# Optimization experiments

Measured on AMD Instinct MI355X. Metric: run time of the kernel, lower is better.

## Reference

```python
import jax, jax.numpy as jnp
import numpy as np

LN_EPS = 1e-5


def setup_inputs() -> dict:
    key = jax.random.key(0)
    ks = jax.random.split(key, 12)
    B, T, C, D, P = 4, 1024, 16, 256, 4096
    s = 1.0 / np.sqrt(D)
    x = jax.random.normal(ks[0], (B, T, C, D), jnp.float32)
    x_mask = jax.random.uniform(ks[1], (B, T, C)) < 0.1
    pos = jax.random.randint(ks[2], (B, T, C), 0, P)
    ang = jax.random.uniform(ks[3], (P, D // 2), minval=-np.pi, maxval=np.pi)
    pe = jnp.stack([jnp.cos(ang), jnp.sin(ang)], axis=-1)  # [P, D/2, 2] unit complex
    wq_w = jax.random.normal(ks[4], (D, D), jnp.float32) * s
    wq_b = jnp.zeros((D,), jnp.float32)
    wk_w = jax.random.normal(ks[5], (D, D), jnp.float32) * s
    wk_b = jnp.zeros((D,), jnp.float32)
    wv_w = jax.random.normal(ks[6], (D, D), jnp.float32) * s
    wv_b = jnp.zeros((D,), jnp.float32)
    ln_g = jnp.ones((D,), jnp.float32)
    ln_b = jnp.zeros((D,), jnp.float32)
    ls_gamma = 1e-5 * jnp.ones((D,), jnp.float32)
    return {"x": x, "x_mask": x_mask, "pos": pos, "pe": pe,
            "wq_w": wq_w, "wq_b": wq_b, "wk_w": wk_w, "wk_b": wk_b,
            "wv_w": wv_w, "wv_b": wv_b, "ln_g": ln_g, "ln_b": ln_b,
            "ls_gamma": ls_gamma}


def _rotate(q, pe, pos):
    # q: [B,T,C,D]; pe: [P,D/2,2]; pos: [B,T,C] -> complex mult q * pe[pos]
    B, T, C, D = q.shape
    qr = q.reshape(B, T, C, D // 2, 2)
    r = pe[pos]  # [B,T,C,D/2,2]
    re = qr[..., 0] * r[..., 0] - qr[..., 1] * r[..., 1]
    im = qr[..., 0] * r[..., 1] + qr[..., 1] * r[..., 0]
    return jnp.stack([re, im], axis=-1).reshape(B, T, C, D)


def reference(x, x_mask, pos, pe, wq_w, wq_b, wk_w, wk_b, wv_w, wv_b, ln_g, ln_b, ls_gamma):
    B, T, C, D = x.shape
    scale = 1.0 / jnp.sqrt(jnp.asarray(D, x.dtype))
    q = jnp.einsum('btcd,ed->btce', x, wq_w) + wq_b
    k = jnp.einsum('btcd,ed->btce', x, wk_w) + wk_b
    v = jnp.einsum('btcd,ed->btce', x, wv_w) + wv_b
    q = _rotate(q, pe, pos)
    k = _rotate(k, pe, pos)
    # (b c) t d layout -> keep as [b,c,t,d]
    q = q.transpose(0, 2, 1, 3)
    k = k.transpose(0, 2, 1, 3)
    v = v.transpose(0, 2, 1, 3)
    attn = jnp.einsum('bcqd,bckd->bcqk', q, k) * scale  # [b,c,tq,tk]
    m = x_mask.transpose(0, 2, 1)  # [b,c,t]
    mask = m[:, :, :, None] | m[:, :, None, :]  # OR-combined pad mask
    attn = jnp.where(mask, jnp.asarray(-1e30, attn.dtype), attn)
    p = jax.nn.softmax(attn, axis=-1)
    # fully masked rows: torch softmax(-inf row)->nan->nan_to_num(0)
    all_masked = jnp.all(mask, axis=-1, keepdims=True)
    p = jnp.where(all_masked, jnp.zeros((), p.dtype), p)
    o = jnp.einsum('bcqk,bckd->bqcd', p, v)  # [b,t,c,d]
    y = x + ls_gamma * o
    mu = y.mean(-1, keepdims=True)
    var = ((y - mu) ** 2).mean(-1, keepdims=True)
    out = (y - mu) / jnp.sqrt(var + LN_EPS) * ln_g + ln_b
    return out
```

## Files before the change

kernel.cpp:

```cpp
#include <hip/hip_runtime.h>


typedef __attribute__((ext_vector_type(8))) short short8_t;
typedef __attribute__((ext_vector_type(4))) short short4_t;
typedef __attribute__((ext_vector_type(8))) float float8_t;
typedef __attribute__((ext_vector_type(4))) float float4_t;
typedef __attribute__((ext_vector_type(2))) float float2_t;

__device__ __forceinline__ float b2f(short s) {
    union { unsigned int u; float f; } x;
    x.u = ((unsigned int)(unsigned short)s) << 16;
    return x.f;
}
__device__ __forceinline__ short f2bt(float f) {
    union { float f; unsigned int u; } x; x.f = f;
    return (short)(x.u >> 16);
}

__device__ __forceinline__ void stage16(const short* g, short* l) {
    __builtin_amdgcn_global_load_lds(
        (const __attribute__((address_space(1))) unsigned int*)g,
        (__attribute__((address_space(3))) unsigned int*)l, 16, 0, 0);
}

__global__ __launch_bounds__(256) void prep_kernel(
    const float* __restrict__ wq, const float* __restrict__ wk,
    const float* __restrict__ wv, const unsigned char* __restrict__ xmask,
    short* __restrict__ wb, float* __restrict__ mbg)
{
    if (blockIdx.x < 192) {
        int idx = blockIdx.x * 256 + threadIdx.x;
        int mat = idx >> 14, off = idx & 16383;
        const float* src = (mat == 0) ? wq : ((mat == 1) ? wk : wv);
        float4_t v = *(const float4_t*)(src + (long)off * 4);
        short4_t o;
#pragma unroll
        for (int j = 0; j < 4; j++) o[j] = f2bt(v[j]);
        *(short4_t*)(wb + (long)idx * 4) = o;
    } else {
        int idx = (blockIdx.x - 192) * 256 + threadIdx.x;
        int bc = idx >> 10, t = idx & 1023;
        int b = bc >> 4, c = bc & 15;
        mbg[idx] = xmask[((long)b * 1024 + t) * 16 + c] ? -1e30f : 0.0f;
    }
}

__global__ __launch_bounds__(256) void qkv_mfma_kernel(
    const float* __restrict__ x, const int* __restrict__ pos,
    const float* __restrict__ pe, const short* __restrict__ wb,
    const float* __restrict__ bq, const float* __restrict__ bk,
    const float* __restrict__ bv,
    short* __restrict__ qo, short* __restrict__ ko, short* __restrict__ vt)
{
    __shared__ __align__(16) short xs[64 * 264];
    __shared__ __align__(16) short ys[18432];
    __shared__ int posb[64];

    const int tid = threadIdx.x;
    const int lane = tid & 63;
    const int wid = tid >> 6;
    const int bc = blockIdx.x >> 4;
    const int t0 = (blockIdx.x & 15) * 64;
    const int b = bc >> 4, c = bc & 15;
    const int row = lane & 15, quad = lane >> 4;
    const int odd = lane & 1;
    const int n0 = wid * 64;
    const long kvbase = (long)bc * 262144;

#pragma unroll
    for (int j = 0; j < 8; j++) {
        int idx = tid + j * 256;
        int r = idx >> 5, c8 = idx & 31;
        const float* xp = x + (((long)b * 1024 + t0 + r) * 16 + c) * 256 + c8 * 8;
        float4_t a = *(const float4_t*)xp;
        float4_t d = *(const float4_t*)(xp + 4);
        short8_t o;
        o[0] = f2bt(a.x); o[1] = f2bt(a.y); o[2] = f2bt(a.z); o[3] = f2bt(a.w);
        o[4] = f2bt(d.x); o[5] = f2bt(d.y); o[6] = f2bt(d.z); o[7] = f2bt(d.w);
        *(short8_t*)&xs[r * 264 + c8 * 8] = o;
    }
    if (tid < 64) posb[tid] = pos[((long)b * 1024 + t0 + tid) * 16 + c];
    __syncthreads();

#pragma unroll 1
    for (int mat = 0; mat < 3; mat++) {
        const short* W = wb + mat * 65536;
        float4_t acc[4][4];
#pragma unroll
        for (int mt = 0; mt < 4; mt++)
#pragma unroll
            for (int nt = 0; nt < 4; nt++) acc[mt][nt] = (float4_t){0.f, 0.f, 0.f, 0.f};

        short8_t Ac[4], Bc[4], An[4], Bn[4];
        auto loadA = [&](short8_t* A, int k0) {
#pragma unroll
            for (int mt = 0; mt < 4; mt++)
                A[mt] = *(const short8_t*)&xs[(mt * 16 + row) * 264 + k0 * 32 + quad * 8];
        };
        auto loadB = [&](short8_t* Bf, int k0) {
#pragma unroll
            for (int nt = 0; nt < 4; nt++)
                Bf[nt] = *(const short8_t*)(W + (n0 + nt * 16 + row) * 256 + k0 * 32 + quad * 8);
        };
        loadA(Ac, 0); loadB(Bc, 0);
#pragma unroll
        for (int k0 = 0; k0 < 8; k0++) {
            if (k0 < 7) { loadA(An, k0 + 1); loadB(Bn, k0 + 1); }
#pragma unroll
            for (int mt = 0; mt < 4; mt++)
#pragma unroll
                for (int nt = 0; nt < 4; nt++)
                    acc[mt][nt] = __builtin_amdgcn_mfma_f32_16x16x32_bf16(
                        Ac[mt], Bc[nt], acc[mt][nt], 0, 0, 0);
            if (k0 < 7) {
#pragma unroll
                for (int i = 0; i < 4; i++) { Ac[i] = An[i]; Bc[i] = Bn[i]; }
            }
        }

        const float* bias = (mat == 0) ? bq : ((mat == 1) ? bk : bv);
        float bs[4];
#pragma unroll
        for (int nt = 0; nt < 4; nt++) bs[nt] = bias[n0 + nt * 16 + row];
#pragma unroll
        for (int mt = 0; mt < 4; mt++)
#pragma unroll
            for (int nt = 0; nt < 4; nt++)
#pragma unroll
                for (int r = 0; r < 4; r++) acc[mt][nt][r] += bs[nt];

        if (mat < 2) {
#pragma unroll
            for (int mt = 0; mt < 4; mt++)
#pragma unroll
                for (int r = 0; r < 4; r++) {
                    int p = posb[mt * 16 + quad * 4 + r];
                    const float* pb = pe + (long)p * 256;
#pragma unroll
                    for (int nt = 0; nt < 4; nt++) {
                        int i = (n0 + nt * 16 + row) >> 1;
                        float2_t cs = *(const float2_t*)(pb + i * 2);
                        float v = acc[mt][nt][r];
                        float pr = __shfl_xor(v, 1);
                        acc[mt][nt][r] = v * cs.x + pr * (odd ? cs.y : -cs.y);
                    }
                }
        }

        __syncthreads();
        if (mat < 2) {
#pragma unroll
            for (int mt = 0; mt < 4; mt++)
#pragma unroll
                for (int nt = 0; nt < 4; nt++) {
                    int n = n0 + nt * 16 + row;
#pragma unroll
                    for (int r = 0; r < 4; r++)
                        ys[(mt * 16 + quad * 4 + r) * 264 + n] = f2bt(acc[mt][nt][r]);
                }
            __syncthreads();
            short* dst = ((mat == 0) ? qo : ko) + kvbase + (long)t0 * 256;
#pragma unroll
            for (int j = 0; j < 8; j++) {
                int idx = tid + j * 256;
                int r = idx >> 5, c8 = idx & 31;
                *(short8_t*)(dst + r * 256 + c8 * 8) = *(const short8_t*)&ys[r * 264 + c8 * 8];
            }
        } else {
#pragma unroll
            for (int mt = 0; mt < 4; mt++)
#pragma unroll
                for (int nt = 0; nt < 4; nt++) {
                    int n = n0 + nt * 16 + row;
                    short4_t o4;
#pragma unroll
                    for (int r = 0; r < 4; r++) o4[r] = f2bt(acc[mt][nt][r]);
                    *(short4_t*)&ys[n * 72 + mt * 16 + quad * 4] = o4;
                }
            __syncthreads();
#pragma unroll
            for (int j = 0; j < 8; j++) {
                int idx = tid + j * 256;
                int d = idx >> 3, t8 = idx & 7;
                *(short8_t*)(vt + kvbase + (long)d * 1024 + t0 + t8 * 8) =
                    *(const short8_t*)&ys[d * 72 + t8 * 8];
            }
        }
    }
}

__global__ __launch_bounds__(512, 2) void attn_kernel(
    const short* __restrict__ qg, const short* __restrict__ kg,
    const short* __restrict__ vt, const float* __restrict__ mbg,
    const float* __restrict__ x,
    const float* __restrict__ lsg, const float* __restrict__ lng,
    const float* __restrict__ lnb, float* __restrict__ out)
{
    __shared__ __align__(16) short lds[56320];

    const int tid = threadIdx.x;
    const int lane = tid & 63;
    const int wid = tid >> 6;
    const int bid = (blockIdx.x & 7) * 64 + (blockIdx.x >> 3);
    const int bc = bid >> 3;
    const int tq0 = (bid & 7) * 128;
    const int b = bc >> 4, c = bc & 15;
    const long kvbase = (long)bc * 262144;
    const int bcq = bc * 1024;
    const int row = lane & 15, quad = lane >> 4;
    float* mbsf = (float*)&lds[54272];

    auto stage = [&](int j, int buf) {
#pragma unroll
        for (int i = 0; i < 2; i++) {
            int rp = (wid * 2 + i) * 2;
            int r = rp + (lane >> 5);
            int slot = lane & 31;
            const short* g = kg + kvbase + (long)(j * 32 + r) * 256 +
                             ((slot ^ (r & 7)) << 3);
            stage16(g, &lds[buf * 8192 + rp * 256]);
        }
#pragma unroll
        for (int i = 0; i < 2; i++) {
            int db = (wid * 2 + i) * 16;
            int d = db + (lane >> 2);
            int slot = lane & 3;
            const short* g = vt + kvbase + (long)d * 1024 + j * 32 +
                             (((slot ^ ((d >> 1) & 3))) << 3);
            stage16(g, &lds[24576 + buf * 8192 + db * 32]);
        }
    };

    stage(0, 0);
    stage(1, 1);
#pragma unroll
    for (int i = tid; i < 1024; i += 512) mbsf[i] = mbg[bcq + i];
    short8_t aq[8];
#pragma unroll
    for (int f = 0; f < 8; f++)
        aq[f] = *(const short8_t*)(qg + kvbase +
            (long)(tq0 + wid * 16 + row) * 256 + f * 32 + quad * 8);

    float4_t oacc[16];
#pragma unroll
    for (int nt = 0; nt < 16; nt++) oacc[nt] = (float4_t){0.f, 0.f, 0.f, 0.f};
    float m[4], lsum[4];
#pragma unroll
    for (int r = 0; r < 4; r++) { m[r] = -__builtin_inff(); lsum[r] = 0.f; }

    const float scale = 0.0625f;
    const int ptw = 49152 + wid * 640 + row * 20 + quad * 4;
    const int prd = 49152 + wid * 640 + quad * 160 + row;

    asm volatile("s_waitcnt lgkmcnt(0)" ::: "memory");

    int bcur = 0;
#pragma unroll 1
    for (int j = 0; j < 32; j++) {
        int bnx = bcur + 2; if (bnx >= 3) bnx -= 3;
        if (j < 30) {
            stage(j + 2, bnx);
            asm volatile("s_waitcnt vmcnt(8)" ::: "memory");
        } else if (j == 30) {
            asm volatile("s_waitcnt vmcnt(4)" ::: "memory");
        } else {
            asm volatile("s_waitcnt vmcnt(0)" ::: "memory");
        }
        __builtin_amdgcn_s_barrier();

        const short* Kb = &lds[bcur * 8192];
        const short* Vb = &lds[24576 + bcur * 8192];

        float4_t s0 = {0.f, 0.f, 0.f, 0.f}, s1 = {0.f, 0.f, 0.f, 0.f};
#pragma unroll
        for (int f = 0; f < 8; f++) {
            short8_t k0 = *(const short8_t*)&Kb[row * 256 + (((f * 4 + quad) ^ (row & 7)) << 3)];
            short8_t k1 = *(const short8_t*)&Kb[(16 + row) * 256 + (((f * 4 + quad) ^ ((16 + row) & 7)) << 3)];
            s0 = __builtin_amdgcn_mfma_f32_16x16x32_bf16(aq[f], k0, s0, 0, 0, 0);
            s1 = __builtin_amdgcn_mfma_f32_16x16x32_bf16(aq[f], k1, s1, 0, 0, 0);
        }
        float mb0 = mbsf[j * 32 + row], mb1 = mbsf[j * 32 + 16 + row];
        float sv[2][4], tm[4];
#pragma unroll
        for (int r = 0; r < 4; r++) {
            sv[0][r] = s0[r] * scale + mb0;
            sv[1][r] = s1[r] * scale + mb1;
            tm[r] = fmaxf(sv[0][r], sv[1][r]);
        }
#pragma unroll
        for (int r = 0; r < 4; r++)
#pragma unroll
            for (int o = 1; o < 16; o <<= 1) tm[r] = fmaxf(tm[r], __shfl_xor(tm[r], o));
        float g = fmaxf(fmaxf(tm[0] - m[0], tm[1] - m[1]),
                        fmaxf(tm[2] - m[2], tm[3] - m[3]));
        if (!__all(g <= 8.f)) {
#pragma unroll
            for (int r = 0; r < 4; r++) {
                float nm = fmaxf(m[r], tm[r]);
                float fac = __expf(m[r] - nm);
                lsum[r] *= fac; m[r] = nm;
#pragma unroll
                for (int nt = 0; nt < 16; nt++) oacc[nt][r] *= fac;
            }
        }
        short4_t p4[2];
#pragma unroll
        for (int h = 0; h < 2; h++)
#pragma unroll
            for (int r = 0; r < 4; r++) {
                float p = __expf(sv[h][r] - m[r]);
                lsum[r] += p;
                p4[h][r] = f2bt(p);
            }
        *(short4_t*)&lds[ptw] = p4[0];
        *(short4_t*)&lds[ptw + 320] = p4[1];
        short8_t pa;
#pragma unroll
        for (int jj = 0; jj < 8; jj++) pa[jj] = lds[prd + jj * 20];

#pragma unroll
        for (int nt = 0; nt < 16; nt++) {
            int d = nt * 16 + row;
            short8_t vbf = *(const short8_t*)&Vb[d * 32 + ((quad ^ ((d >> 1) & 3)) << 3)];
            oacc[nt] = __builtin_amdgcn_mfma_f32_16x16x32_bf16(pa, vbf, oacc[nt], 0, 0, 0);
        }

        asm volatile("s_waitcnt lgkmcnt(0)" ::: "memory");
        __builtin_amdgcn_s_barrier();
        bcur++; if (bcur >= 3) bcur = 0;
    }

    float inv[4];
#pragma unroll
    for (int r = 0; r < 4; r++) {
        float s = lsum[r];
#pragma unroll
        for (int o = 1; o < 16; o <<= 1) s += __shfl_xor(s, o);
        int qi = tq0 + wid * 16 + quad * 4 + r;
        inv[r] = (mbsf[qi] != 0.f) ? 0.f : (1.f / s);
    }
    long xb[4];
#pragma unroll
    for (int r = 0; r < 4; r++)
        xb[r] = (((long)b * 1024 + tq0 + wid * 16 + quad * 4 + r) * 16 + c) * 256 + row;

    float s1r[4] = {0.f, 0.f, 0.f, 0.f}, s2r[4] = {0.f, 0.f, 0.f, 0.f};
#pragma unroll
    for (int nt = 0; nt < 16; nt++) {
        int d = nt * 16 + row;
        float lg = lsg[d];
#pragma unroll
        for (int r = 0; r < 4; r++) {
            float yy = x[xb[r] + nt * 16] + lg * (oacc[nt][r] * inv[r]);
            oacc[nt][r] = yy;
            s1r[r] += yy; s2r[r] += yy * yy;
        }
    }
    float mu[4], rstd[4];
#pragma unroll
    for (int r = 0; r < 4; r++) {
#pragma unroll
        for (int o = 1; o < 16; o <<= 1) {
            s1r[r] += __shfl_xor(s1r[r], o);
            s2r[r] += __shfl_xor(s2r[r], o);
        }
        mu[r] = s1r[r] * (1.f / 256.f);
        float var = s2r[r] * (1.f / 256.f) - mu[r] * mu[r];
        rstd[r] = rsqrtf(var + 1e-5f);
    }
#pragma unroll
    for (int nt = 0; nt < 16; nt++) {
        int d = nt * 16 + row;
        float g2 = lng[d], b2 = lnb[d];
#pragma unroll
        for (int r = 0; r < 4; r++)
            out[xb[r] + nt * 16] = (oacc[nt][r] - mu[r]) * rstd[r] * g2 + b2;
    }
}

extern "C" void kernel_launch(void* const* d_in, const int* in_sizes, int n_in,
                              void* d_out, int out_size, void* d_ws, size_t ws_size,
                              hipStream_t stream) {
    const float* x = (const float*)d_in[0];
    const unsigned char* xmask = (const unsigned char*)d_in[1];
    const int* pos = (const int*)d_in[2];
    const float* pe = (const float*)d_in[3];
    const float* wq = (const float*)d_in[4];
    const float* bq = (const float*)d_in[5];
    const float* wk = (const float*)d_in[6];
    const float* bk = (const float*)d_in[7];
    const float* wv = (const float*)d_in[8];
    const float* bv = (const float*)d_in[9];
    const float* lng = (const float*)d_in[10];
    const float* lnb = (const float*)d_in[11];
    const float* lsg = (const float*)d_in[12];
    float* out = (float*)d_out;

    short* qw = (short*)d_ws;
    short* kw = qw + 16777216;
    short* vtw = kw + 16777216;
    short* wbw = vtw + 16777216;
    float* mbg = (float*)(wbw + 196608);

    prep_kernel<<<448, 256, 0, stream>>>(wq, wk, wv, xmask, wbw, mbg);
    qkv_mfma_kernel<<<1024, 256, 0, stream>>>(x, pos, pe, wbw, bq, bk, bv,
                                              qw, kw, vtw);
    attn_kernel<<<512, 512, 0, stream>>>(qw, kw, vtw, mbg, x, lsg, lng, lnb, out);
}
```

Baseline: 354.9 us.

## Process two 16-row query tiles per wave to reuse K/V tiles

Each wave now computes attention for 32 query rows (two MFMA M-tiles) against each staged K/V block, and each block covers 256 queries, halving the grid. This doubles arithmetic per LDS load of K and V and halves total K/V staging from global memory. It doubles accumulator and softmax state registers, which may cause spills or lower occupancy, and leaves fewer blocks to spread across the GPU.

```diff
diff --git a/kernel.cpp b/kernel.cpp
--- a/kernel.cpp
+++ b/kernel.cpp
@@ -196,19 +196,19 @@
     const float* __restrict__ lsg, const float* __restrict__ lng,
     const float* __restrict__ lnb, float* __restrict__ out)
 {
-    __shared__ __align__(16) short lds[56320];
+    __shared__ __align__(16) short lds[59904];
 
     const int tid = threadIdx.x;
     const int lane = tid & 63;
     const int wid = tid >> 6;
-    const int bid = (blockIdx.x & 7) * 64 + (blockIdx.x >> 3);
-    const int bc = bid >> 3;
-    const int tq0 = (bid & 7) * 128;
+    const int bid = (blockIdx.x & 7) * 32 + (blockIdx.x >> 3);
+    const int bc = bid >> 2;
+    const int tq0 = (bid & 3) * 256;
     const int b = bc >> 4, c = bc & 15;
     const long kvbase = (long)bc * 262144;
     const int bcq = bc * 1024;
     const int row = lane & 15, quad = lane >> 4;
-    float* mbsf = (float*)&lds[54272];
+    float* mbsf = (float*)&lds[57856];
 
     auto stage = [&](int j, int buf) {
 #pragma unroll
@@ -235,22 +235,27 @@
     stage(1, 1);
 #pragma unroll
     for (int i = tid; i < 1024; i += 512) mbsf[i] = mbg[bcq + i];
-    short8_t aq[8];
-#pragma unroll
-    for (int f = 0; f < 8; f++)
-        aq[f] = *(const short8_t*)(qg + kvbase +
-            (long)(tq0 + wid * 16 + row) * 256 + f * 32 + quad * 8);
-
-    float4_t oacc[16];
-#pragma unroll
-    for (int nt = 0; nt < 16; nt++) oacc[nt] = (float4_t){0.f, 0.f, 0.f, 0.f};
-    float m[4], lsum[4];
-#pragma unroll
-    for (int r = 0; r < 4; r++) { m[r] = -__builtin_inff(); lsum[r] = 0.f; }
+    short8_t aq[2][8];
+#pragma unroll
+    for (int mt = 0; mt < 2; mt++)
+#pragma unroll
+        for (int f = 0; f < 8; f++)
+            aq[mt][f] = *(const short8_t*)(qg + kvbase +
+                (long)(tq0 + wid * 32 + mt * 16 + row) * 256 + f * 32 + quad * 8);
+
+    float4_t oacc[2][16];
+#pragma unroll
+    for (int mt = 0; mt < 2; mt++)
+#pragma unroll
+        for (int nt = 0; nt < 16; nt++) oacc[mt][nt] = (float4_t){0.f, 0.f, 0.f, 0.f};
+    float m[2][4], lsum[2][4];
+#pragma unroll
+    for (int mt = 0; mt < 2; mt++)
+#pragma unroll
+        for (int r = 0; r < 4; r++) { m[mt][r] = -__builtin_inff(); lsum[mt][r] = 0.f; }
 
     const float scale = 0.0625f;
-    const int ptw = 49152 + wid * 640 + row * 20 + quad * 4;
-    const int prd = 49152 + wid * 640 + quad * 160 + row;
+    const int PTB = 49152 + wid * 1088;
 
     asm volatile("s_waitcnt lgkmcnt(0)" ::: "memory");
 
@@ -271,58 +276,80 @@
         const short* Kb = &lds[bcur * 8192];
         const short* Vb = &lds[24576 + bcur * 8192];
 
-        float4_t s0 = {0.f, 0.f, 0.f, 0.f}, s1 = {0.f, 0.f, 0.f, 0.f};
+        float4_t s00 = {0.f,0.f,0.f,0.f}, s01 = {0.f,0.f,0.f,0.f};
+        float4_t s10 = {0.f,0.f,0.f,0.f}, s11 = {0.f,0.f,0.f,0.f};
 #pragma unroll
         for (int f = 0; f < 8; f++) {
             short8_t k0 = *(const short8_t*)&Kb[row * 256 + (((f * 4 + quad) ^ (row & 7)) << 3)];
             short8_t k1 = *(const short8_t*)&Kb[(16 + row) * 256 + (((f * 4 + quad) ^ ((16 + row) & 7)) << 3)];
-            s0 = __builtin_amdgcn_mfma_f32_16x16x32_bf16(aq[f], k0, s0, 0, 0, 0);
-            s1 = __builtin_amdgcn_mfma_f32_16x16x32_bf16(aq[f], k1, s1, 0, 0, 0);
+            s00 = __builtin_amdgcn_mfma_f32_16x16x32_bf16(aq[0][f], k0, s00, 0, 0, 0);
+            s01 = __builtin_amdgcn_mfma_f32_16x16x32_bf16(aq[0][f], k1, s01, 0, 0, 0);
+            s10 = __builtin_amdgcn_mfma_f32_16x16x32_bf16(aq[1][f], k0, s10, 0, 0, 0);
+            s11 = __builtin_amdgcn_mfma_f32_16x16x32_bf16(aq[1][f], k1, s11, 0, 0, 0);
         }
         float mb0 = mbsf[j * 32 + row], mb1 = mbsf[j * 32 + 16 + row];
-        float sv[2][4], tm[4];
+        float tm[2][4];
 #pragma unroll
         for (int r = 0; r < 4; r++) {
-            sv[0][r] = s0[r] * scale + mb0;
-            sv[1][r] = s1[r] * scale + mb1;
-            tm[r] = fmaxf(sv[0][r], sv[1][r]);
-        }
-#pragma unroll
-        for (int r = 0; r < 4; r++)
-#pragma unroll
-            for (int o = 1; o < 16; o <<= 1) tm[r] = fmaxf(tm[r], __shfl_xor(tm[r], o));
-        float g = fmaxf(fmaxf(tm[0] - m[0], tm[1] - m[1]),
-                        fmaxf(tm[2] - m[2], tm[3] - m[3]));
+            s00[r] = s00[r] * scale + mb0;  s01[r] = s01[r] * scale + mb1;
+            s10[r] = s10[r] * scale + mb0;  s11[r] = s11[r] * scale + mb1;
+            tm[0][r] = fmaxf(s00[r], s01[r]);
+            tm[1][r] = fmaxf(s10[r], s11[r]);
+        }
+#pragma unroll
+        for (int mt = 0; mt < 2; mt++)
+#pragma unroll
+            for (int r = 0; r < 4; r++)
+#pragma unroll
+                for (int o = 1; o < 16; o <<= 1)
+                    tm[mt][r] = fmaxf(tm[mt][r], __shfl_xor(tm[mt][r], o));
+        float g = fmaxf(
+            fmaxf(fmaxf(tm[0][0] - m[0][0], tm[0][1] - m[0][1]),
+                  fmaxf(tm[0][2] - m[0][2], tm[0][3] - m[0][3])),
+            fmaxf(fmaxf(tm[1][0] - m[1][0], tm[1][1] - m[1][1]),
+                  fmaxf(tm[1][2] - m[1][2], tm[1][3] - m[1][3])));
         if (!__all(g <= 8.f)) {
 #pragma unroll
+            for (int mt = 0; mt < 2; mt++)
+#pragma unroll
+                for (int r = 0; r < 4; r++) {
+                    float nm = fmaxf(m[mt][r], tm[mt][r]);
+                    float fac = __expf(m[mt][r] - nm);
+                    lsum[mt][r] *= fac; m[mt][r] = nm;
+#pragma unroll
+                    for (int nt = 0; nt < 16; nt++) oacc[mt][nt][r] *= fac;
+                }
+        }
+        {
+            short4_t pk0, pk1;
+#pragma unroll
             for (int r = 0; r < 4; r++) {
-                float nm = fmaxf(m[r], tm[r]);
-                float fac = __expf(m[r] - nm);
-                lsum[r] *= fac; m[r] = nm;
-#pragma unroll
-                for (int nt = 0; nt < 16; nt++) oacc[nt][r] *= fac;
-            }
-        }
-        short4_t p4[2];
-#pragma unroll
-        for (int h = 0; h < 2; h++)
+                float p0 = __expf(s00[r] - m[0][r]); lsum[0][r] += p0; pk0[r] = f2bt(p0);
+                float p1 = __expf(s01[r] - m[0][r]); lsum[0][r] += p1; pk1[r] = f2bt(p1);
+            }
+            *(short4_t*)&lds[PTB + row * 34 + quad * 4] = pk0;
+            *(short4_t*)&lds[PTB + (16 + row) * 34 + quad * 4] = pk1;
 #pragma unroll
             for (int r = 0; r < 4; r++) {
-                float p = __expf(sv[h][r] - m[r]);
-                lsum[r] += p;
-                p4[h][r] = f2bt(p);
-            }
-        *(short4_t*)&lds[ptw] = p4[0];
-        *(short4_t*)&lds[ptw + 320] = p4[1];
-        short8_t pa;
-#pragma unroll
-        for (int jj = 0; jj < 8; jj++) pa[jj] = lds[prd + jj * 20];
+                float p0 = __expf(s10[r] - m[1][r]); lsum[1][r] += p0; pk0[r] = f2bt(p0);
+                float p1 = __expf(s11[r] - m[1][r]); lsum[1][r] += p1; pk1[r] = f2bt(p1);
+            }
+            *(short4_t*)&lds[PTB + row * 34 + 16 + quad * 4] = pk0;
+            *(short4_t*)&lds[PTB + (16 + row) * 34 + 16 + quad * 4] = pk1;
+        }
+        short8_t pa[2];
+#pragma unroll
+        for (int mt = 0; mt < 2; mt++)
+#pragma unroll
+            for (int jj = 0; jj < 8; jj++)
+                pa[mt][jj] = lds[PTB + (quad * 8 + jj) * 34 + mt * 16 + row];
 
 #pragma unroll
         for (int nt = 0; nt < 16; nt++) {
             int d = nt * 16 + row;
             short8_t vbf = *(const short8_t*)&Vb[d * 32 + ((quad ^ ((d >> 1) & 3)) << 3)];
-            oacc[nt] = __builtin_amdgcn_mfma_f32_16x16x32_bf16(pa, vbf, oacc[nt], 0, 0, 0);
+            oacc[0][nt] = __builtin_amdgcn_mfma_f32_16x16x32_bf16(pa[0], vbf, oacc[0][nt], 0, 0, 0);
+            oacc[1][nt] = __builtin_amdgcn_mfma_f32_16x16x32_bf16(pa[1], vbf, oacc[1][nt], 0, 0, 0);
         }
 
         asm volatile("s_waitcnt lgkmcnt(0)" ::: "memory");
@@ -330,51 +357,62 @@
         bcur++; if (bcur >= 3) bcur = 0;
     }
 
-    float inv[4];
-#pragma unroll
-    for (int r = 0; r < 4; r++) {
-        float s = lsum[r];
-#pragma unroll
-        for (int o = 1; o < 16; o <<= 1) s += __shfl_xor(s, o);
-        int qi = tq0 + wid * 16 + quad * 4 + r;
-        inv[r] = (mbsf[qi] != 0.f) ? 0.f : (1.f / s);
-    }
-    long xb[4];
-#pragma unroll
-    for (int r = 0; r < 4; r++)
-        xb[r] = (((long)b * 1024 + tq0 + wid * 16 + quad * 4 + r) * 16 + c) * 256 + row;
-
-    float s1r[4] = {0.f, 0.f, 0.f, 0.f}, s2r[4] = {0.f, 0.f, 0.f, 0.f};
+    float inv[2][4];
+#pragma unroll
+    for (int mt = 0; mt < 2; mt++)
+#pragma unroll
+        for (int r = 0; r < 4; r++) {
+            float s = lsum[mt][r];
+#pragma unroll
+            for (int o = 1; o < 16; o <<= 1) s += __shfl_xor(s, o);
+            int qi = tq0 + wid * 32 + mt * 16 + quad * 4 + r;
+            inv[mt][r] = (mbsf[qi] != 0.f) ? 0.f : (1.f / s);
+        }
+    long xb[2][4];
+#pragma unroll
+    for (int mt = 0; mt < 2; mt++)
+#pragma unroll
+        for (int r = 0; r < 4; r++)
+            xb[mt][r] = (((long)b * 1024 + tq0 + wid * 32 + mt * 16 + quad * 4 + r) * 16 + c) * 256 + row;
+
+    float s1r[2][4] = {{0.f,0.f,0.f,0.f},{0.f,0.f,0.f,0.f}};
+    float s2r[2][4] = {{0.f,0.f,0.f,0.f},{0.f,0.f,0.f,0.f}};
 #pragma unroll
     for (int nt = 0; nt < 16; nt++) {
         int d = nt * 16 + row;
         float lg = lsg[d];
 #pragma unroll
+        for (int mt = 0; mt < 2; mt++)
+#pragma unroll
+            for (int r = 0; r < 4; r++) {
+                float yy = x[xb[mt][r] + nt * 16] + lg * (oacc[mt][nt][r] * inv[mt][r]);
+                oacc[mt][nt][r] = yy;
+                s1r[mt][r] += yy; s2r[mt][r] += yy * yy;
+            }
+    }
+    float mu[2][4], rstd[2][4];
+#pragma unroll
+    for (int mt = 0; mt < 2; mt++)
+#pragma unroll
         for (int r = 0; r < 4; r++) {
-            float yy = x[xb[r] + nt * 16] + lg * (oacc[nt][r] * inv[r]);
-            oacc[nt][r] = yy;
-            s1r[r] += yy; s2r[r] += yy * yy;
-        }
-    }
-    float mu[4], rstd[4];
-#pragma unroll
-    for (int r = 0; r < 4; r++) {
-#pragma unroll
-        for (int o = 1; o < 16; o <<= 1) {
-            s1r[r] += __shfl_xor(s1r[r], o);
-            s2r[r] += __shfl_xor(s2r[r], o);
-        }
-        mu[r] = s1r[r] * (1.f / 256.f);
-        float var = s2r[r] * (1.f / 256.f) - mu[r] * mu[r];
-        rstd[r] = rsqrtf(var + 1e-5f);
-    }
+#pragma unroll
+            for (int o = 1; o < 16; o <<= 1) {
+                s1r[mt][r] += __shfl_xor(s1r[mt][r], o);
+                s2r[mt][r] += __shfl_xor(s2r[mt][r], o);
+            }
+            mu[mt][r] = s1r[mt][r] * (1.f / 256.f);
+            float var = s2r[mt][r] * (1.f / 256.f) - mu[mt][r] * mu[mt][r];
+            rstd[mt][r] = rsqrtf(var + 1e-5f);
+        }
 #pragma unroll
     for (int nt = 0; nt < 16; nt++) {
         int d = nt * 16 + row;
         float g2 = lng[d], b2 = lnb[d];
 #pragma unroll
-        for (int r = 0; r < 4; r++)
-            out[xb[r] + nt * 16] = (oacc[nt][r] - mu[r]) * rstd[r] * g2 + b2;
+        for (int mt = 0; mt < 2; mt++)
+#pragma unroll
+            for (int r = 0; r < 4; r++)
+                out[xb[mt][r] + nt * 16] = (oacc[mt][nt][r] - mu[mt][r]) * rstd[mt][r] * g2 + b2;
     }
 }
 
@@ -405,5 +443,5 @@
     prep_kernel<<<448, 256, 0, stream>>>(wq, wk, wv, xmask, wbw, mbg);
     qkv_mfma_kernel<<<1024, 256, 0, stream>>>(x, pos, pe, wbw, bq, bk, bv,
                                               qw, kw, vtw);
-    attn_kernel<<<512, 512, 0, stream>>>(qw, kw, vtw, mbg, x, lsg, lng, lnb, out);
-}
+    attn_kernel<<<256, 512, 0, stream>>>(qw, kw, vtw, mbg, x, lsg, lng, lnb, out);
+}
```

Result: slower. 390.6 us (+10.1%).
